# Performance work log

Hardware: AMD Instinct MI355X
Metric: run time of the kernel (lower is better)

Reference implementation:

```python
import jax, jax.numpy as jnp
import numpy as np

H = 16
D_MODEL = 1024
D_K = D_MODEL // H  # 64, must equal embeddim


def setup_inputs() -> dict:
    key = jax.random.key(0)
    ks = jax.random.split(key, 20)
    B, S, D = 4, 1024, D_MODEL
    s = 0.02
    inp = {
        'query': jax.random.normal(ks[0], (B, S, D), jnp.float32),
        'key':   jax.random.normal(ks[1], (B, S, D), jnp.float32),
        'value': jax.random.normal(ks[2], (B, S, D), jnp.float32),
        'mask':  jnp.ones((B, S, S), jnp.int32),
        # four d_model x d_model projections (q, k, v, out)
        'wq': jax.random.normal(ks[3], (D, D), jnp.float32) * s, 'bq': jnp.zeros((D,), jnp.float32),
        'wk': jax.random.normal(ks[4], (D, D), jnp.float32) * s, 'bk': jnp.zeros((D,), jnp.float32),
        'wv': jax.random.normal(ks[5], (D, D), jnp.float32) * s, 'bv': jnp.zeros((D,), jnp.float32),
        'wo': jax.random.normal(ks[6], (D, D), jnp.float32) * s, 'bo': jnp.zeros((D,), jnp.float32),
        # per-head (embeddim=64) linears
        'spatial_w': jax.random.normal(ks[7], (D_K, D_K), jnp.float32) * s, 'spatial_b': jnp.zeros((D_K,), jnp.float32),
        'qproj_w':   jax.random.normal(ks[8], (D_K, D_K), jnp.float32) * s, 'qproj_b':   jnp.zeros((D_K,), jnp.float32),
        'kproj_w':   jax.random.normal(ks[9], (D_K, D_K), jnp.float32) * s, 'kproj_b':   jnp.zeros((D_K,), jnp.float32),
        'vlin_w':    jax.random.normal(ks[10], (D_K, D_K), jnp.float32) * s, 'vlin_b':    jnp.zeros((D_K,), jnp.float32),
        # channel_linear: Linear(1, 64)
        'chan_w': jax.random.normal(ks[11], (1, D_K), jnp.float32) * s, 'chan_b': jnp.zeros((D_K,), jnp.float32),
    }
    return inp


def reference(query, key, value, mask,
              wq, bq, wk, bk, wv, bv, wo, bo,
              spatial_w, spatial_b, qproj_w, qproj_b,
              kproj_w, kproj_b, vlin_w, vlin_b, chan_w, chan_b):
    B, S, D = query.shape
    # project and split heads -> [B, H, S, D_K]
    def heads(x, w, b):
        return (x @ w + b).reshape(B, S, H, D_K).transpose(0, 2, 1, 3)
    q = heads(query, wq, bq)
    k = heads(key, wk, bk)
    v = heads(value, wv, bv)

    q = jax.nn.elu(q @ spatial_w + spatial_b)
    q_refine = q @ qproj_w + qproj_b
    # channel gate: mean over channels -> Linear(1,64) -> matmul with raw key
    alpha = q_refine.mean(-1, keepdims=True) @ chan_w + chan_b        # [B,H,S,64]
    gate = jax.nn.sigmoid(jnp.einsum('bhqe,bhke->bhqk', alpha, k))    # [B,H,S,S]

    k2 = jax.nn.elu(k @ kproj_w + kproj_b)
    scores = jnp.einsum('bhqe,bhke->bhqk', q, k2) / jnp.sqrt(jnp.asarray(D_K, q.dtype))
    scores = scores * gate
    scores = jnp.where(mask[:, None] == 0, jnp.asarray(-1e9, scores.dtype), scores)
    p_attn = jax.nn.softmax(scores, axis=-1)

    v2 = jax.nn.elu(v @ vlin_w + vlin_b)
    x = jnp.einsum('bhqk,bhke->bhqe', p_attn, v2)                     # [B,H,S,64]
    x = x.transpose(0, 2, 1, 3).reshape(B, S, H * D_K)
    return x @ wo + bo
```

## Files before the change

### kernel.cpp

```cpp
#include <hip/hip_runtime.h>
#include <math.h>

#define D_MODEL 1024
#define NH 16
#define DK 64
#define S_LEN 1024
#define BATCH 4
#define MROWS (BATCH * S_LEN)

typedef short bf16x8 __attribute__((ext_vector_type(8)));
typedef float f32x4 __attribute__((ext_vector_type(4)));
typedef unsigned short u16;

__device__ __forceinline__ float elu1(float x) {
    return x > 0.f ? x : (expf(x) - 1.f);
}

__device__ __forceinline__ u16 f2bf(float f) {
    union { float f; unsigned u; } v; v.f = f;
    unsigned u = v.u;
    return (u16)((u + 0x7fffu + ((u >> 16) & 1u)) >> 16);
}

__device__ __forceinline__ unsigned pack2(float a, float b) {
    union { float f; unsigned u; } ua, ub; ua.f = a; ub.f = b;
    return ((ua.u + 0x8000u) >> 16) | ((ub.u + 0x8000u) & 0xffff0000u);
}

__device__ __forceinline__ void async16(const void* g, void* l) {
    __builtin_amdgcn_global_load_lds(
        (const __attribute__((address_space(1))) unsigned int*)g,
        (__attribute__((address_space(3))) unsigned int*)l,
        16, 0, 0);
}

__global__ __launch_bounds__(256) void cast_wt(
    const float* __restrict__ wq, const float* __restrict__ wk,
    const float* __restrict__ wv, const float* __restrict__ wo,
    u16* __restrict__ WT)
{
    __shared__ float T[64][65];
    const int z = blockIdx.z;
    const float* W = (z == 0) ? wq : ((z == 1) ? wk : ((z == 2) ? wv : wo));
    u16* O = WT + (size_t)z * D_MODEL * D_MODEL;
    const int tid = threadIdx.x;
    const int k0 = blockIdx.y * 64, n0 = blockIdx.x * 64;
    const int r = tid >> 4, c4 = (tid & 15) * 4;
    #pragma unroll
    for (int p = 0; p < 4; p++) {
        float4 v = *(const float4*)&W[(size_t)(k0 + r + p * 16) * D_MODEL + n0 + c4];
        T[r + p * 16][c4 + 0] = v.x; T[r + p * 16][c4 + 1] = v.y;
        T[r + p * 16][c4 + 2] = v.z; T[r + p * 16][c4 + 3] = v.w;
    }
    __syncthreads();
    #pragma unroll
    for (int p = 0; p < 4; p++) {
        const int i = r + p * 16;
        ushort4 o4;
        o4.x = f2bf(T[c4 + 0][i]); o4.y = f2bf(T[c4 + 1][i]);
        o4.z = f2bf(T[c4 + 2][i]); o4.w = f2bf(T[c4 + 3][i]);
        *(ushort4*)&O[(size_t)(n0 + i) * D_MODEL + k0 + c4] = o4;
    }
}

__global__ __launch_bounds__(256) void proj_fused(
    const float* __restrict__ Xq, const float* __restrict__ Xk, const float* __restrict__ Xv,
    const u16* __restrict__ WTq, const u16* __restrict__ WTk, const u16* __restrict__ WTv,
    const float* __restrict__ bq, const float* __restrict__ bk, const float* __restrict__ bv,
    const float* __restrict__ spatial_w, const float* __restrict__ spatial_b,
    const float* __restrict__ qproj_w, const float* __restrict__ qproj_b,
    const float* __restrict__ kproj_w, const float* __restrict__ kproj_b,
    const float* __restrict__ vlin_w, const float* __restrict__ vlin_b,
    const float* __restrict__ chan_w, const float* __restrict__ chan_b,
    u16* __restrict__ Qh, u16* __restrict__ K2, u16* __restrict__ V2t,
    float* __restrict__ mB, float* __restrict__ uB, float* __restrict__ vB)
{
    __shared__ __align__(16) u16 smem[23040];
    __shared__ float auxA[64];
    __shared__ float auxS;

    u16* As = smem;
    u16* Bs = smem + 4096;
    u16* W2t = smem + 18432;

    const int z = blockIdx.z;
    const float* X = (z == 0) ? Xq : ((z == 1) ? Xk : Xv);
    const u16* WT = (z == 0) ? WTq : ((z == 1) ? WTk : WTv);
    const float* B1 = (z == 0) ? bq : ((z == 1) ? bk : bv);
    const float* W2 = (z == 0) ? spatial_w : ((z == 1) ? kproj_w : vlin_w);
    const float* B2 = (z == 0) ? spatial_b : ((z == 1) ? kproj_b : vlin_b);

    const int tid = threadIdx.x;
    const int wave = tid >> 6, lane = tid & 63;
    const int col = lane & 15, quad = lane >> 4;
    const int wr = wave >> 1, wc = wave & 1;
    const int n0 = blockIdx.x * 128, r0 = blockIdx.y * 128;
    const int hh = blockIdx.x * 2 + wc;

    #pragma unroll
    for (int p = 0; p < 4; p++) {
        int idx = p * 256 + tid;
        int f = idx >> 4, e4 = (idx & 15) * 4;
        float4 w4 = *(const float4*)&W2[f * 64 + e4];
        W2t[(e4 + 0) * 72 + f] = f2bf(w4.x);
        W2t[(e4 + 1) * 72 + f] = f2bf(w4.y);
        W2t[(e4 + 2) * 72 + f] = f2bf(w4.z);
        W2t[(e4 + 3) * 72 + f] = f2bf(w4.w);
    }
    if (z == 0) {
        {
            int row = tid >> 2, part = tid & 3;
            float s = 0.f;
            for (int e = part * 16; e < part * 16 + 16; e++) s += qproj_w[row * 64 + e];
            s += __shfl_xor(s, 1);
            s += __shfl_xor(s, 2);
            if (part == 0) auxA[row] = s * (1.f / 64.f);
        }
        if (tid < 64) {
            float s = qproj_b[tid];
            #pragma unroll
            for (int m = 1; m < 64; m <<= 1) s += __shfl_xor(s, m);
            if (tid == 0) auxS = s * (1.f / 64.f);
        }
    }

    const int arow = tid >> 1, ahalf = tid & 1;
    const float* aptr = X + (size_t)(r0 + arow) * D_MODEL + ahalf * 16;
    u16* adst = As + arow * 32 + ahalf * 16;

    const int ch0 = 2 * wave, ch1 = 2 * wave + 1;
    const u16* bptr0 = WT + (size_t)(n0 + ch0 * 16 + (lane >> 2)) * D_MODEL + (lane & 3) * 8;
    const u16* bptr1 = WT + (size_t)(n0 + ch1 * 16 + (lane >> 2)) * D_MODEL + (lane & 3) * 8;
    u16* bdst0 = Bs + ch0 * 512;
    u16* bdst1 = Bs + ch1 * 512;

    f32x4 acc[4][4];
    #pragma unroll
    for (int i = 0; i < 4; i++)
        #pragma unroll
        for (int j = 0; j < 4; j++)
            acc[i][j] = (f32x4){0.f, 0.f, 0.f, 0.f};

    float4 f0 = *(const float4*)(aptr);
    float4 f1 = *(const float4*)(aptr + 4);
    float4 f2 = *(const float4*)(aptr + 8);
    float4 f3 = *(const float4*)(aptr + 12);

    for (int k0 = 0; k0 < D_MODEL; k0 += 32) {
        if (k0) __syncthreads();
        async16(bptr0 + k0, bdst0);
        async16(bptr1 + k0, bdst1);
        {
            uint4 p0, p1;
            p0.x = pack2(f0.x, f0.y); p0.y = pack2(f0.z, f0.w);
            p0.z = pack2(f1.x, f1.y); p0.w = pack2(f1.z, f1.w);
            p1.x = pack2(f2.x, f2.y); p1.y = pack2(f2.z, f2.w);
            p1.z = pack2(f3.x, f3.y); p1.w = pack2(f3.z, f3.w);
            *(uint4*)adst = p0;
            *(uint4*)(adst + 8) = p1;
        }
        if (k0 + 32 < D_MODEL) {
            const float* ap = aptr + k0 + 32;
            f0 = *(const float4*)(ap);
            f1 = *(const float4*)(ap + 4);
            f2 = *(const float4*)(ap + 8);
            f3 = *(const float4*)(ap + 12);
        }
        __syncthreads();
        const u16* Ab = As + (wr * 64 + col) * 32 + quad * 8;
        const u16* Bb = Bs + (wc * 64 + col) * 32 + quad * 8;
        bf16x8 af[4], bfr[4];
        #pragma unroll
        for (int mi = 0; mi < 4; mi++) af[mi] = *(const bf16x8*)(Ab + mi * 512);
        #pragma unroll
        for (int ni = 0; ni < 4; ni++) bfr[ni] = *(const bf16x8*)(Bb + ni * 512);
        #pragma unroll
        for (int mi = 0; mi < 4; mi++)
            #pragma unroll
            for (int ni = 0; ni < 4; ni++)
                acc[mi][ni] = __builtin_amdgcn_mfma_f32_16x16x32_bf16(af[mi], bfr[ni], acc[mi][ni], 0, 0, 0);
    }

    float b1v[4];
    #pragma unroll
    for (int ni = 0; ni < 4; ni++) b1v[ni] = B1[hh * 64 + ni * 16 + col];

    const int rbase = r0 + wr * 64;
    const int b = rbase >> 10;
    const int s0 = rbase & 1023;
    const size_t svecbase = ((size_t)b * NH + hh) * S_LEN;

    if (z == 1) {
        float cw[4], cb[4];
        #pragma unroll
        for (int ni = 0; ni < 4; ni++) { cw[ni] = chan_w[ni * 16 + col]; cb[ni] = chan_b[ni * 16 + col]; }
        #pragma unroll
        for (int mi = 0; mi < 4; mi++)
            #pragma unroll
            for (int r = 0; r < 4; r++) {
                float su = 0.f, sv = 0.f;
                #pragma unroll
                for (int ni = 0; ni < 4; ni++) {
                    float p = acc[mi][ni][r] + b1v[ni];
                    su += p * cw[ni];
                    sv += p * cb[ni];
                }
                su += __shfl_xor(su, 1); su += __shfl_xor(su, 2);
                su += __shfl_xor(su, 4); su += __shfl_xor(su, 8);
                sv += __shfl_xor(sv, 1); sv += __shfl_xor(sv, 2);
                sv += __shfl_xor(sv, 4); sv += __shfl_xor(sv, 8);
                if (col == 0) {
                    const size_t idx = svecbase + s0 + mi * 16 + quad * 4 + r;
                    uB[idx] = su;
                    vB[idx] = sv;
                }
            }
    }

    __syncthreads();

    u16* Pw = smem + wave * 4608;
    #pragma unroll
    for (int mi = 0; mi < 4; mi++)
        #pragma unroll
        for (int ni = 0; ni < 4; ni++)
            #pragma unroll
            for (int r = 0; r < 4; r++)
                Pw[(mi * 16 + quad * 4 + r) * 72 + ni * 16 + col] =
                    f2bf(acc[mi][ni][r] + b1v[ni]);

    __builtin_amdgcn_s_waitcnt(0xc07f);

    bf16x8 af2[4][2], bf2r[4][2];
    #pragma unroll
    for (int mi = 0; mi < 4; mi++) {
        af2[mi][0] = *(const bf16x8*)&Pw[(mi * 16 + col) * 72 + quad * 8];
        af2[mi][1] = *(const bf16x8*)&Pw[(mi * 16 + col) * 72 + 32 + quad * 8];
    }
    #pragma unroll
    for (int ni = 0; ni < 4; ni++) {
        bf2r[ni][0] = *(const bf16x8*)&W2t[(ni * 16 + col) * 72 + quad * 8];
        bf2r[ni][1] = *(const bf16x8*)&W2t[(ni * 16 + col) * 72 + 32 + quad * 8];
    }
    f32x4 out2[4][4];
    #pragma unroll
    for (int mi = 0; mi < 4; mi++)
        #pragma unroll
        for (int ni = 0; ni < 4; ni++) {
            f32x4 c = (f32x4){0.f, 0.f, 0.f, 0.f};
            c = __builtin_amdgcn_mfma_f32_16x16x32_bf16(af2[mi][0], bf2r[ni][0], c, 0, 0, 0);
            c = __builtin_amdgcn_mfma_f32_16x16x32_bf16(af2[mi][1], bf2r[ni][1], c, 0, 0, 0);
            out2[mi][ni] = c;
        }

    float b2v[4];
    #pragma unroll
    for (int ni = 0; ni < 4; ni++) b2v[ni] = B2[ni * 16 + col];
    float qs[4][4][4];
    #pragma unroll
    for (int mi = 0; mi < 4; mi++)
        #pragma unroll
        for (int ni = 0; ni < 4; ni++)
            #pragma unroll
            for (int r = 0; r < 4; r++)
                qs[mi][ni][r] = elu1(out2[mi][ni][r] + b2v[ni]);

    if (z == 0) {
        float aw[4];
        #pragma unroll
        for (int ni = 0; ni < 4; ni++) aw[ni] = auxA[ni * 16 + col];
        #pragma unroll
        for (int mi = 0; mi < 4; mi++)
            #pragma unroll
            for (int r = 0; r < 4; r++) {
                float pm = 0.f;
                #pragma unroll
                for (int ni = 0; ni < 4; ni++) pm += qs[mi][ni][r] * aw[ni];
                pm += __shfl_xor(pm, 1); pm += __shfl_xor(pm, 2);
                pm += __shfl_xor(pm, 4); pm += __shfl_xor(pm, 8);
                if (col == 0)
                    mB[svecbase + s0 + mi * 16 + quad * 4 + r] = pm + auxS;
            }
        #pragma unroll
        for (int mi = 0; mi < 4; mi++)
            #pragma unroll
            for (int ni = 0; ni < 4; ni++)
                #pragma unroll
                for (int r = 0; r < 4; r++)
                    Qh[(size_t)(rbase + mi * 16 + quad * 4 + r) * D_MODEL
                       + hh * 64 + ni * 16 + col] = f2bf(qs[mi][ni][r] * 0.125f);
    } else if (z == 1) {
        #pragma unroll
        for (int mi = 0; mi < 4; mi++)
            #pragma unroll
            for (int ni = 0; ni < 4; ni++)
                #pragma unroll
                for (int r = 0; r < 4; r++)
                    K2[(size_t)(rbase + mi * 16 + quad * 4 + r) * D_MODEL
                       + hh * 64 + ni * 16 + col] = f2bf(qs[mi][ni][r]);
    } else {
        __builtin_amdgcn_s_waitcnt(0xc07f);
        #pragma unroll
        for (int mi = 0; mi < 4; mi++)
            #pragma unroll
            for (int ni = 0; ni < 4; ni++)
                #pragma unroll
                for (int r = 0; r < 4; r++)
                    Pw[(ni * 16 + col) * 72 + mi * 16 + quad * 4 + r] = f2bf(qs[mi][ni][r]);
        __builtin_amdgcn_s_waitcnt(0xc07f);
        const int d = lane;
        u16* dst = V2t + (((size_t)b * NH + hh) * DK + d) * S_LEN + s0;
        const u16* srcp = Pw + d * 72;
        #pragma unroll
        for (int seg = 0; seg < 8; seg++)
            *(uint4*)(dst + seg * 8) = *(const uint4*)(srcp + seg * 8);
    }
}

__global__ __launch_bounds__(256) void attn_mfma(
    const u16* __restrict__ Qh, const u16* __restrict__ K2h, const u16* __restrict__ V2t,
    const float* __restrict__ Mq, const float* __restrict__ Uk, const float* __restrict__ Vk,
    const int* __restrict__ mask, u16* __restrict__ X)
{
    __shared__ u16 K2s[2][64][72];
    __shared__ u16 V2s[64][72];

    const int tid = threadIdx.x;
    const int wave = tid >> 6, lane = tid & 63;
    const int col = lane & 15, quad = lane >> 4;
    const int b = blockIdx.z, h = blockIdx.y;
    const int q0 = blockIdx.x * 64;
    const size_t hb = ((size_t)(b * NH + h)) * S_LEN * DK;
    const size_t sb = ((size_t)(b * NH + h)) * S_LEN;

    bf16x8 qf0, qf1;
    {
        const u16* qp = Qh + (size_t)(b * S_LEN + q0 + wave * 16 + col) * D_MODEL + h * 64 + quad * 8;
        qf0 = *(const bf16x8*)qp;
        qf1 = *(const bf16x8*)(qp + 32);
    }
    float mqv[4];
    #pragma unroll
    for (int r = 0; r < 4; r++)
        mqv[r] = Mq[sb + q0 + wave * 16 + quad * 4 + r];

    const int srow = tid >> 2, sseg = tid & 3;
    const u16* ksrc = K2h + (size_t)(b * S_LEN + srow) * D_MODEL + h * 64 + sseg * 16;
    const u16* vsrc = V2t + hb + (size_t)srow * S_LEN + sseg * 16;
    const int* mrow = mask + (size_t)b * S_LEN * S_LEN
                    + (size_t)(q0 + wave * 16 + quad * 4) * S_LEN + col;

    uint4 ka = *(const uint4*)(ksrc);
    uint4 kb = *(const uint4*)(ksrc + 8);
    uint4 va = *(const uint4*)(vsrc);
    uint4 vb = *(const uint4*)(vsrc + 8);
    float ku[4], kv[4];
    int mk[4][4];
    #pragma unroll
    for (int nb = 0; nb < 4; nb++) {
        ku[nb] = Uk[sb + nb * 16 + col];
        kv[nb] = Vk[sb + nb * 16 + col];
        #pragma unroll
        for (int r = 0; r < 4; r++) mk[nb][r] = mrow[(size_t)r * S_LEN + nb * 16];
    }

    float psum[4] = {0.f, 0.f, 0.f, 0.f};
    f32x4 o[4];
    #pragma unroll
    for (int nb = 0; nb < 4; nb++) o[nb] = (f32x4){0.f, 0.f, 0.f, 0.f};

    for (int t = 0; t < 16; t++) {
        const int bsel = t & 1;
        *(uint4*)&K2s[bsel][srow][sseg * 16]     = ka;
        *(uint4*)&K2s[bsel][srow][sseg * 16 + 8] = kb;
        *(uint4*)&V2s[srow][sseg * 16]           = va;
        *(uint4*)&V2s[srow][sseg * 16 + 8]       = vb;
        __syncthreads();

        float kun[4], kvn[4];
        int mkn[4][4];
        if (t < 15) {
            const int k1 = (t + 1) * 64;
            const u16* ks = ksrc + (size_t)k1 * D_MODEL;
            const u16* vs = vsrc + k1;
            ka = *(const uint4*)(ks);
            kb = *(const uint4*)(ks + 8);
            va = *(const uint4*)(vs);
            vb = *(const uint4*)(vs + 8);
            #pragma unroll
            for (int nb = 0; nb < 4; nb++) {
                kun[nb] = Uk[sb + k1 + nb * 16 + col];
                kvn[nb] = Vk[sb + k1 + nb * 16 + col];
                #pragma unroll
                for (int r = 0; r < 4; r++)
                    mkn[nb][r] = mrow[k1 + (size_t)r * S_LEN + nb * 16];
            }
        }

        f32x4 sc[4];
        #pragma unroll
        for (int nb = 0; nb < 4; nb++) {
            bf16x8 b0 = *(const bf16x8*)&K2s[bsel][nb * 16 + col][quad * 8];
            bf16x8 b1 = *(const bf16x8*)&K2s[bsel][nb * 16 + col][32 + quad * 8];
            f32x4 c = (f32x4){0.f, 0.f, 0.f, 0.f};
            c = __builtin_amdgcn_mfma_f32_16x16x32_bf16(qf0, b0, c, 0, 0, 0);
            c = __builtin_amdgcn_mfma_f32_16x16x32_bf16(qf1, b1, c, 0, 0, 0);
            sc[nb] = c;
        }

        u16* Ps = &K2s[1 - bsel][wave * 16][0];
        #pragma unroll
        for (int nb = 0; nb < 4; nb++) {
            #pragma unroll
            for (int r = 0; r < 4; r++) {
                float g = 1.f / (1.f + __expf(-(mqv[r] * ku[nb] + kv[nb])));
                float sv = sc[nb][r] * g;
                sv = mk[nb][r] ? sv : -30.f;
                float p = __expf(sv);
                psum[r] += p;
                Ps[(quad * 4 + r) * 72 + nb * 16 + col] = f2bf(p);
            }
        }
        __builtin_amdgcn_s_waitcnt(0xc07f);
        bf16x8 a0 = *(const bf16x8*)&Ps[col * 72 + quad * 8];
        bf16x8 a1 = *(const bf16x8*)&Ps[col * 72 + 32 + quad * 8];

        #pragma unroll
        for (int nb = 0; nb < 4; nb++) {
            bf16x8 b0 = *(const bf16x8*)&V2s[nb * 16 + col][quad * 8];
            bf16x8 b1 = *(const bf16x8*)&V2s[nb * 16 + col][32 + quad * 8];
            o[nb] = __builtin_amdgcn_mfma_f32_16x16x32_bf16(a0, b0, o[nb], 0, 0, 0);
            o[nb] = __builtin_amdgcn_mfma_f32_16x16x32_bf16(a1, b1, o[nb], 0, 0, 0);
        }
        __syncthreads();

        if (t < 15) {
            #pragma unroll
            for (int nb = 0; nb < 4; nb++) {
                ku[nb] = kun[nb]; kv[nb] = kvn[nb];
                #pragma unroll
                for (int r = 0; r < 4; r++) mk[nb][r] = mkn[nb][r];
            }
        }
    }

    #pragma unroll
    for (int r = 0; r < 4; r++) {
        float t = psum[r];
        t += __shfl_xor(t, 1);
        t += __shfl_xor(t, 2);
        t += __shfl_xor(t, 4);
        t += __shfl_xor(t, 8);
        float inv = 1.f / t;
        u16* xp = X + (size_t)(b * S_LEN + q0 + wave * 16 + quad * 4 + r) * D_MODEL + h * 64 + col;
        #pragma unroll
        for (int nb = 0; nb < 4; nb++)
            xp[nb * 16] = f2bf(o[nb][r] * inv);
    }
}

__global__ __launch_bounds__(256) void out_gemm(
    const u16* __restrict__ A, const u16* __restrict__ WT,
    const float* __restrict__ bias, float* __restrict__ C)
{
    __shared__ u16 As[128 * 32];
    __shared__ u16 Bs[128 * 32];

    const int tid = threadIdx.x;
    const int wave = tid >> 6, lane = tid & 63;
    const int col = lane & 15, quad = lane >> 4;
    const int wr = wave >> 1, wc = wave & 1;
    const int n0 = blockIdx.x * 128, r0 = blockIdx.y * 128;

    const int ch0 = 2 * wave, ch1 = 2 * wave + 1;
    const u16* aptr0 = A + (size_t)(r0 + ch0 * 16 + (lane >> 2)) * D_MODEL + (lane & 3) * 8;
    const u16* aptr1 = A + (size_t)(r0 + ch1 * 16 + (lane >> 2)) * D_MODEL + (lane & 3) * 8;
    const u16* bptr0 = WT + (size_t)(n0 + ch0 * 16 + (lane >> 2)) * D_MODEL + (lane & 3) * 8;
    const u16* bptr1 = WT + (size_t)(n0 + ch1 * 16 + (lane >> 2)) * D_MODEL + (lane & 3) * 8;
    u16* adst0 = As + ch0 * 512;
    u16* adst1 = As + ch1 * 512;
    u16* bdst0 = Bs + ch0 * 512;
    u16* bdst1 = Bs + ch1 * 512;

    f32x4 acc[4][4];
    #pragma unroll
    for (int i = 0; i < 4; i++)
        #pragma unroll
        for (int j = 0; j < 4; j++)
            acc[i][j] = (f32x4){0.f, 0.f, 0.f, 0.f};

    for (int k0 = 0; k0 < D_MODEL; k0 += 32) {
        if (k0) __syncthreads();
        async16(aptr0 + k0, adst0);
        async16(aptr1 + k0, adst1);
        async16(bptr0 + k0, bdst0);
        async16(bptr1 + k0, bdst1);
        __syncthreads();
        const u16* Ab = As + (wr * 64 + col) * 32 + quad * 8;
        const u16* Bb = Bs + (wc * 64 + col) * 32 + quad * 8;
        bf16x8 af[4], bfr[4];
        #pragma unroll
        for (int mi = 0; mi < 4; mi++) af[mi] = *(const bf16x8*)(Ab + mi * 512);
        #pragma unroll
        for (int ni = 0; ni < 4; ni++) bfr[ni] = *(const bf16x8*)(Bb + ni * 512);
        #pragma unroll
        for (int mi = 0; mi < 4; mi++)
            #pragma unroll
            for (int ni = 0; ni < 4; ni++)
                acc[mi][ni] = __builtin_amdgcn_mfma_f32_16x16x32_bf16(af[mi], bfr[ni], acc[mi][ni], 0, 0, 0);
    }

    #pragma unroll
    for (int mi = 0; mi < 4; mi++)
        #pragma unroll
        for (int ni = 0; ni < 4; ni++) {
            const int gr = r0 + wr * 64 + mi * 16 + quad * 4;
            const int gc = n0 + wc * 64 + ni * 16 + col;
            const float bb = bias[gc];
            #pragma unroll
            for (int r = 0; r < 4; r++)
                C[(size_t)(gr + r) * D_MODEL + gc] = acc[mi][ni][r] + bb;
        }
}

extern "C" void kernel_launch(void* const* d_in, const int* in_sizes, int n_in,
                              void* d_out, int out_size, void* d_ws, size_t ws_size,
                              hipStream_t stream) {
    (void)in_sizes; (void)n_in; (void)out_size; (void)ws_size;
    const float* query = (const float*)d_in[0];
    const float* key_  = (const float*)d_in[1];
    const float* value = (const float*)d_in[2];
    const int*   mask  = (const int*)d_in[3];
    const float* wq = (const float*)d_in[4];  const float* bq = (const float*)d_in[5];
    const float* wk = (const float*)d_in[6];  const float* bk = (const float*)d_in[7];
    const float* wv = (const float*)d_in[8];  const float* bv = (const float*)d_in[9];
    const float* wo = (const float*)d_in[10]; const float* bo = (const float*)d_in[11];
    const float* spatial_w = (const float*)d_in[12]; const float* spatial_b = (const float*)d_in[13];
    const float* qproj_w   = (const float*)d_in[14]; const float* qproj_b   = (const float*)d_in[15];
    const float* kproj_w   = (const float*)d_in[16]; const float* kproj_b   = (const float*)d_in[17];
    const float* vlin_w    = (const float*)d_in[18]; const float* vlin_b    = (const float*)d_in[19];
    const float* chan_w    = (const float*)d_in[20]; const float* chan_b    = (const float*)d_in[21];
    float* out = (float*)d_out;

    char* ws = (char*)d_ws;
    u16* Qh  = (u16*)ws;
    u16* K2  = (u16*)(ws + ((size_t)8  << 20));
    u16* Xb  = (u16*)(ws + ((size_t)16 << 20));
    u16* WT  = (u16*)(ws + ((size_t)24 << 20));
    u16* V2t = (u16*)(ws + ((size_t)32 << 20));
    float* mB = (float*)(ws + ((size_t)40 << 20));
    float* uB = mB + (size_t)BATCH * NH * S_LEN;
    float* vB = uB + (size_t)BATCH * NH * S_LEN;
    const size_t WSZ = (size_t)D_MODEL * D_MODEL;

    cast_wt<<<dim3(16, 16, 4), 256, 0, stream>>>(wq, wk, wv, wo, WT);
    proj_fused<<<dim3(8, 32, 3), 256, 0, stream>>>(query, key_, value,
        WT, WT + WSZ, WT + 2 * WSZ, bq, bk, bv,
        spatial_w, spatial_b, qproj_w, qproj_b, kproj_w, kproj_b,
        vlin_w, vlin_b, chan_w, chan_b,
        Qh, K2, V2t, mB, uB, vB);
    attn_mfma<<<dim3(S_LEN / 64, NH, BATCH), 256, 0, stream>>>(Qh, K2, V2t, mB, uB, vB, mask, Xb);
    out_gemm<<<dim3(8, 32), 256, 0, stream>>>(Xb, WT + 3 * WSZ, bo, out);
}
```

Before: 330.4 us.

## Widen projection K-step, double-buffer attention V tiles, swap GEMM grid order

The fused projection GEMM now stages 64-wide K slices per iteration (two 32-wide halves), halving the number of barrier pairs. The attention kernel double-buffers the V tile and gives P its own per-wave shared buffer, which removes the trailing barrier of each KV iteration. Both GEMM kernels swap grid dimensions so consecutive blocks walk rows while sharing the same weight column block, which may improve L2 reuse of the weights. In exchange, shared-memory use and register pressure in the attention and projection kernels rise, which could lower occupancy.

```diff
diff --git a/kernel.cpp b/kernel.cpp
--- a/kernel.cpp
+++ b/kernel.cpp
@@ -80,7 +80,7 @@
     __shared__ float auxS;
 
     u16* As = smem;
-    u16* Bs = smem + 4096;
+    u16* Bs = smem + 8192;
     u16* W2t = smem + 18432;
 
     const int z = blockIdx.z;
@@ -94,8 +94,8 @@
     const int wave = tid >> 6, lane = tid & 63;
     const int col = lane & 15, quad = lane >> 4;
     const int wr = wave >> 1, wc = wave & 1;
-    const int n0 = blockIdx.x * 128, r0 = blockIdx.y * 128;
-    const int hh = blockIdx.x * 2 + wc;
+    const int r0 = blockIdx.x * 128, n0 = blockIdx.y * 128;
+    const int hh = blockIdx.y * 2 + wc;
 
     #pragma unroll
     for (int p = 0; p < 4; p++) {
@@ -124,15 +124,16 @@
         }
     }
 
-    const int arow = tid >> 1, ahalf = tid & 1;
-    const float* aptr = X + (size_t)(r0 + arow) * D_MODEL + ahalf * 16;
-    u16* adst = As + arow * 32 + ahalf * 16;
-
-    const int ch0 = 2 * wave, ch1 = 2 * wave + 1;
-    const u16* bptr0 = WT + (size_t)(n0 + ch0 * 16 + (lane >> 2)) * D_MODEL + (lane & 3) * 8;
-    const u16* bptr1 = WT + (size_t)(n0 + ch1 * 16 + (lane >> 2)) * D_MODEL + (lane & 3) * 8;
-    u16* bdst0 = Bs + ch0 * 512;
-    u16* bdst1 = Bs + ch1 * 512;
+    const int arow = tid >> 1, ap = tid & 1;
+    const float* aptr = X + (size_t)(r0 + arow) * D_MODEL + ap * 32;
+    u16* adst = As + ap * 4096 + arow * 32;
+
+    const int brow = lane >> 2, bseg = lane & 3;
+    const u16* bp = WT + (size_t)(n0 + wave * 32 + brow) * D_MODEL + bseg * 8;
+    u16* bd_l0 = Bs + (wave * 32) * 32;
+    u16* bd_l1 = Bs + (wave * 32 + 16) * 32;
+    u16* bd_h0 = Bs + 4096 + (wave * 32) * 32;
+    u16* bd_h1 = Bs + 4096 + (wave * 32 + 16) * 32;
 
     f32x4 acc[4][4];
     #pragma unroll
@@ -141,44 +142,48 @@
         for (int j = 0; j < 4; j++)
             acc[i][j] = (f32x4){0.f, 0.f, 0.f, 0.f};
 
-    float4 f0 = *(const float4*)(aptr);
-    float4 f1 = *(const float4*)(aptr + 4);
-    float4 f2 = *(const float4*)(aptr + 8);
-    float4 f3 = *(const float4*)(aptr + 12);
-
-    for (int k0 = 0; k0 < D_MODEL; k0 += 32) {
+    float4 fr[8];
+    #pragma unroll
+    for (int i = 0; i < 8; i++) fr[i] = *(const float4*)(aptr + i * 4);
+
+    for (int k0 = 0; k0 < D_MODEL; k0 += 64) {
         if (k0) __syncthreads();
-        async16(bptr0 + k0, bdst0);
-        async16(bptr1 + k0, bdst1);
+        async16(bp + k0, bd_l0);
+        async16(bp + 16 * D_MODEL + k0, bd_l1);
+        async16(bp + k0 + 32, bd_h0);
+        async16(bp + 16 * D_MODEL + k0 + 32, bd_h1);
         {
-            uint4 p0, p1;
-            p0.x = pack2(f0.x, f0.y); p0.y = pack2(f0.z, f0.w);
-            p0.z = pack2(f1.x, f1.y); p0.w = pack2(f1.z, f1.w);
-            p1.x = pack2(f2.x, f2.y); p1.y = pack2(f2.z, f2.w);
-            p1.z = pack2(f3.x, f3.y); p1.w = pack2(f3.z, f3.w);
-            *(uint4*)adst = p0;
-            *(uint4*)(adst + 8) = p1;
-        }
-        if (k0 + 32 < D_MODEL) {
-            const float* ap = aptr + k0 + 32;
-            f0 = *(const float4*)(ap);
-            f1 = *(const float4*)(ap + 4);
-            f2 = *(const float4*)(ap + 8);
-            f3 = *(const float4*)(ap + 12);
+            #pragma unroll
+            for (int j = 0; j < 4; j++) {
+                uint4 q;
+                q.x = pack2(fr[2 * j].x, fr[2 * j].y);
+                q.y = pack2(fr[2 * j].z, fr[2 * j].w);
+                q.z = pack2(fr[2 * j + 1].x, fr[2 * j + 1].y);
+                q.w = pack2(fr[2 * j + 1].z, fr[2 * j + 1].w);
+                *(uint4*)(adst + j * 8) = q;
+            }
+        }
+        if (k0 + 64 < D_MODEL) {
+            const float* apn = aptr + k0 + 64;
+            #pragma unroll
+            for (int i = 0; i < 8; i++) fr[i] = *(const float4*)(apn + i * 4);
         }
         __syncthreads();
-        const u16* Ab = As + (wr * 64 + col) * 32 + quad * 8;
-        const u16* Bb = Bs + (wc * 64 + col) * 32 + quad * 8;
-        bf16x8 af[4], bfr[4];
-        #pragma unroll
-        for (int mi = 0; mi < 4; mi++) af[mi] = *(const bf16x8*)(Ab + mi * 512);
-        #pragma unroll
-        for (int ni = 0; ni < 4; ni++) bfr[ni] = *(const bf16x8*)(Bb + ni * 512);
-        #pragma unroll
-        for (int mi = 0; mi < 4; mi++)
-            #pragma unroll
-            for (int ni = 0; ni < 4; ni++)
-                acc[mi][ni] = __builtin_amdgcn_mfma_f32_16x16x32_bf16(af[mi], bfr[ni], acc[mi][ni], 0, 0, 0);
+        const u16* Abase = As + (wr * 64 + col) * 32 + quad * 8;
+        const u16* Bbase = Bs + (wc * 64 + col) * 32 + quad * 8;
+        #pragma unroll
+        for (int p = 0; p < 2; p++) {
+            bf16x8 af[4], bfr[4];
+            #pragma unroll
+            for (int mi = 0; mi < 4; mi++) af[mi] = *(const bf16x8*)(Abase + p * 4096 + mi * 512);
+            #pragma unroll
+            for (int ni = 0; ni < 4; ni++) bfr[ni] = *(const bf16x8*)(Bbase + p * 4096 + ni * 512);
+            #pragma unroll
+            for (int mi = 0; mi < 4; mi++)
+                #pragma unroll
+                for (int ni = 0; ni < 4; ni++)
+                    acc[mi][ni] = __builtin_amdgcn_mfma_f32_16x16x32_bf16(af[mi], bfr[ni], acc[mi][ni], 0, 0, 0);
+        }
     }
 
     float b1v[4];
@@ -323,7 +328,8 @@
     const int* __restrict__ mask, u16* __restrict__ X)
 {
     __shared__ u16 K2s[2][64][72];
-    __shared__ u16 V2s[64][72];
+    __shared__ u16 V2s[2][64][72];
+    __shared__ u16 Ps[4][16][72];
 
     const int tid = threadIdx.x;
     const int wave = tid >> 6, lane = tid & 63;
@@ -373,8 +379,8 @@
         const int bsel = t & 1;
         *(uint4*)&K2s[bsel][srow][sseg * 16]     = ka;
         *(uint4*)&K2s[bsel][srow][sseg * 16 + 8] = kb;
-        *(uint4*)&V2s[srow][sseg * 16]           = va;
-        *(uint4*)&V2s[srow][sseg * 16 + 8]       = vb;
+        *(uint4*)&V2s[bsel][srow][sseg * 16]     = va;
+        *(uint4*)&V2s[bsel][srow][sseg * 16 + 8] = vb;
         __syncthreads();
 
         float kun[4], kvn[4];
@@ -408,7 +414,6 @@
             sc[nb] = c;
         }
 
-        u16* Ps = &K2s[1 - bsel][wave * 16][0];
         #pragma unroll
         for (int nb = 0; nb < 4; nb++) {
             #pragma unroll
@@ -418,21 +423,20 @@
                 sv = mk[nb][r] ? sv : -30.f;
                 float p = __expf(sv);
                 psum[r] += p;
-                Ps[(quad * 4 + r) * 72 + nb * 16 + col] = f2bf(p);
+                Ps[wave][quad * 4 + r][nb * 16 + col] = f2bf(p);
             }
         }
         __builtin_amdgcn_s_waitcnt(0xc07f);
-        bf16x8 a0 = *(const bf16x8*)&Ps[col * 72 + quad * 8];
-        bf16x8 a1 = *(const bf16x8*)&Ps[col * 72 + 32 + quad * 8];
+        bf16x8 a0 = *(const bf16x8*)&Ps[wave][col][quad * 8];
+        bf16x8 a1 = *(const bf16x8*)&Ps[wave][col][32 + quad * 8];
 
         #pragma unroll
         for (int nb = 0; nb < 4; nb++) {
-            bf16x8 b0 = *(const bf16x8*)&V2s[nb * 16 + col][quad * 8];
-            bf16x8 b1 = *(const bf16x8*)&V2s[nb * 16 + col][32 + quad * 8];
+            bf16x8 b0 = *(const bf16x8*)&V2s[bsel][nb * 16 + col][quad * 8];
+            bf16x8 b1 = *(const bf16x8*)&V2s[bsel][nb * 16 + col][32 + quad * 8];
             o[nb] = __builtin_amdgcn_mfma_f32_16x16x32_bf16(a0, b0, o[nb], 0, 0, 0);
             o[nb] = __builtin_amdgcn_mfma_f32_16x16x32_bf16(a1, b1, o[nb], 0, 0, 0);
         }
-        __syncthreads();
 
         if (t < 15) {
             #pragma unroll
@@ -470,7 +474,7 @@
     const int wave = tid >> 6, lane = tid & 63;
     const int col = lane & 15, quad = lane >> 4;
     const int wr = wave >> 1, wc = wave & 1;
-    const int n0 = blockIdx.x * 128, r0 = blockIdx.y * 128;
+    const int r0 = blockIdx.x * 128, n0 = blockIdx.y * 128;
 
     const int ch0 = 2 * wave, ch1 = 2 * wave + 1;
     const u16* aptr0 = A + (size_t)(r0 + ch0 * 16 + (lane >> 2)) * D_MODEL + (lane & 3) * 8;
@@ -554,11 +558,11 @@
     const size_t WSZ = (size_t)D_MODEL * D_MODEL;
 
     cast_wt<<<dim3(16, 16, 4), 256, 0, stream>>>(wq, wk, wv, wo, WT);
-    proj_fused<<<dim3(8, 32, 3), 256, 0, stream>>>(query, key_, value,
+    proj_fused<<<dim3(32, 8, 3), 256, 0, stream>>>(query, key_, value,
         WT, WT + WSZ, WT + 2 * WSZ, bq, bk, bv,
         spatial_w, spatial_b, qproj_w, qproj_b, kproj_w, kproj_b,
         vlin_w, vlin_b, chan_w, chan_b,
         Qh, K2, V2t, mB, uB, vB);
     attn_mfma<<<dim3(S_LEN / 64, NH, BATCH), 256, 0, stream>>>(Qh, K2, V2t, mB, uB, vB, mask, Xb);
-    out_gemm<<<dim3(8, 32), 256, 0, stream>>>(Xb, WT + 3 * WSZ, bo, out);
-}
+    out_gemm<<<dim3(32, 8), 256, 0, stream>>>(Xb, WT + 3 * WSZ, bo, out);
+}
```

After: 317.3 us. -3.9%, faster.
